# Performance work log

Measured on AMD Instinct MI355X. Metric: run time of the kernel, lower is better.

The kernel has to match this reference:

```python
import jax, jax.numpy as jnp
from jax import lax
import numpy as np

B, S, D = 32, 2048, 512

def setup_inputs() -> dict:
    key = jax.random.key(0)
    ks = jax.random.split(key, 9)
    inv = 1.0 / np.sqrt(D).astype(np.float32)
    return {
        "query": jax.random.normal(ks[0], (B, 1, D), jnp.float32),
        "value": jax.random.normal(ks[1], (B, S, D), jnp.float32),
        "last_alignment_energy": jax.random.uniform(ks[2], (B, S), jnp.float32),
        "conv_w": jax.random.normal(ks[3], (D, 1, 3), jnp.float32) * 0.1,  # Conv1d(1->D,k=3)
        "conv_b": jax.random.normal(ks[4], (D,), jnp.float32) * 0.01,
        "w_q": jax.random.normal(ks[5], (D, D), jnp.float32) * inv,  # applied as x @ w_q
        "w_v": jax.random.normal(ks[6], (D, D), jnp.float32) * inv,
        "bias": jax.random.uniform(ks[7], (D,), jnp.float32, minval=-0.1, maxval=0.1),
        "score_w": jax.random.normal(ks[8], (D,), jnp.float32) * inv,  # score_proj weight (out=1)
        "score_b": jnp.zeros((), jnp.float32),
    }


def reference(query, value, last_alignment_energy, conv_w, conv_b, w_q, w_v, bias, score_w, score_b):
    # location features: Conv1d(1->D, k=3, pad=1) over the previous alignment
    loc = lax.conv_general_dilated(
        last_alignment_energy[:, None, :], conv_w,
        window_strides=(1,), padding=[(1, 1)],
        dimension_numbers=("NCH", "OIH", "NCH"))  # [B, D, S]
    loc = jnp.transpose(loc, (0, 2, 1)) + conv_b  # [B, S, D]

    # additive attention energy: tanh(Wq q + Wv v + loc + b) @ score_w
    hidden = jnp.tanh(query @ w_q + value @ w_v + loc + bias)  # [B, S, D] (query broadcasts over S)
    scores = hidden @ score_w + score_b                          # [B, S]
    align = jax.nn.softmax(scores, axis=-1)                      # [B, S]

    # context = align^T V
    context = jnp.einsum("bs,bsd->bd", align, value)             # [B, D]
    return context, align
```

## Files before the change

### kernel.cpp

```cpp
#include <hip/hip_runtime.h>
#include <hip/hip_bf16.h>

#define B_ 32
#define S_ 2048
#define D_ 512
#define M_ (B_*S_)

typedef __bf16 bf16x8 __attribute__((ext_vector_type(8)));
typedef float  f32x4  __attribute__((ext_vector_type(4)));

__device__ __forceinline__ float tanh_fast(float x){
  float e2 = __expf(2.f * x);
  return 1.f - 2.f * __builtin_amdgcn_rcpf(e2 + 1.f);
}

__global__ void k_prep(const float* __restrict__ wv,
                       unsigned short* __restrict__ wvr,
                       const float* __restrict__ q,
                       const float* __restrict__ wq,
                       const float* __restrict__ bias,
                       float* __restrict__ qp){
  __shared__ float qs[D_];
  __shared__ float red2[2][128];
  int bid = blockIdx.x, t = threadIdx.x;
  if (bid < 128){
    int frag = bid*4 + (t>>6);
    int lane = t & 63;
    int ks = frag >> 5, nt = frag & 31;
    int k0 = ks*32 + (lane>>4)*8;
    int d  = nt*16 + (lane&15);
    bf16x8 v;
    #pragma unroll
    for (int j=0;j<8;++j) v[j] = (__bf16)wv[(k0+j)*D_ + d];
    *reinterpret_cast<uint4*>(wvr + ((size_t)frag*64 + lane)*8) =
        __builtin_bit_cast(uint4, v);
  } else {
    int idx = bid - 128;
    int b = idx >> 2, ch = idx & 3;
    int dl = t & 127, eg = t >> 7;
    int d  = ch*128 + dl;
    for (int e=t; e<D_; e+=256) qs[e] = q[b*D_+e];
    __syncthreads();
    float a = 0.f;
    #pragma unroll 8
    for (int i=0;i<256;++i){
      int e = eg*256 + i;
      a = fmaf(qs[e], wq[(size_t)e*D_+d], a);
    }
    red2[eg][dl] = a;
    __syncthreads();
    if (eg == 0) qp[b*D_+d] = red2[0][dl] + red2[1][dl] + bias[d];
  }
}

__launch_bounds__(256, 2)
__global__ void k_energy(const float* __restrict__ value,
                         const unsigned short* __restrict__ wvr,
                         const float* __restrict__ qp,
                         const float* __restrict__ energy,
                         const float* __restrict__ conv_w,
                         const float* __restrict__ conv_b,
                         const float* __restrict__ score_w,
                         float* __restrict__ sp,
                         float* __restrict__ cpart,
                         float* __restrict__ mArr,
                         float* __restrict__ lArr){
  const int t    = threadIdx.x;
  const int wave = t >> 6;
  const int lane = t & 63;
  const int quad = lane >> 4;
  const int lm   = lane & 15;
  const int row0 = blockIdx.x * 64;
  const int b    = row0 >> 11;
  const int s0   = row0 & (S_-1);

  __shared__ __align__(16) unsigned short As[2][2][4][64][8];

  const int sr  = t >> 2;
  const int so  = t & 3;
  const float* gA = value + (size_t)(row0+sr)*D_ + so*8;
  unsigned short* wA = &As[0][0][sr>>4][so*16 + (sr&15)][0];

  f32x4 acc[4][8];
  #pragma unroll
  for (int mt=0;mt<4;++mt)
    #pragma unroll
    for (int nt=0;nt<8;++nt)
      acc[mt][nt] = (f32x4){0.f,0.f,0.f,0.f};

  const unsigned short* bP = wvr + ((size_t)(wave*8)*64 + lane)*8;

  bf16x8 bcur[8], bnxt[8];
  #pragma unroll
  for (int n=0;n<8;++n)
    bcur[n] = __builtin_bit_cast(bf16x8,
        *reinterpret_cast<const uint4*>(bP + (size_t)n*512));
  {
    f32x4 p0 = *reinterpret_cast<const f32x4*>(gA);
    f32x4 p1 = *reinterpret_cast<const f32x4*>(gA + 4);
    f32x4 p2 = *reinterpret_cast<const f32x4*>(gA + 32);
    f32x4 p3 = *reinterpret_cast<const f32x4*>(gA + 36);
    bf16x8 t0, t1;
    t0[0]=(__bf16)p0[0]; t0[1]=(__bf16)p0[1]; t0[2]=(__bf16)p0[2]; t0[3]=(__bf16)p0[3];
    t0[4]=(__bf16)p1[0]; t0[5]=(__bf16)p1[1]; t0[6]=(__bf16)p1[2]; t0[7]=(__bf16)p1[3];
    t1[0]=(__bf16)p2[0]; t1[1]=(__bf16)p2[1]; t1[2]=(__bf16)p2[2]; t1[3]=(__bf16)p2[3];
    t1[4]=(__bf16)p3[0]; t1[5]=(__bf16)p3[1]; t1[6]=(__bf16)p3[2]; t1[7]=(__bf16)p3[3];
    *reinterpret_cast<uint4*>(wA)        = __builtin_bit_cast(uint4, t0);
    *reinterpret_cast<uint4*>(wA + 2048) = __builtin_bit_cast(uint4, t1);
  }
  __syncthreads();

  for (int p=0; p<8; ++p){
    const int buf = p & 1;
    unsigned short* wAp = wA + (buf^1)*4096;

    f32x4 n0, n1, n2, n3;
    if (p < 7){
      const float* g = gA + (p+1)*64;
      n0 = *reinterpret_cast<const f32x4*>(g);
      n1 = *reinterpret_cast<const f32x4*>(g + 4);
      n2 = *reinterpret_cast<const f32x4*>(g + 32);
      n3 = *reinterpret_cast<const f32x4*>(g + 36);
    }

    #pragma unroll
    for (int n=0;n<8;++n)
      bnxt[n] = __builtin_bit_cast(bf16x8,
          *reinterpret_cast<const uint4*>(bP + (size_t)((2*p+1)*32+n)*512));

    {
      bf16x8 a[4];
      #pragma unroll
      for (int mt=0;mt<4;++mt)
        a[mt] = *reinterpret_cast<const bf16x8*>(&As[buf][0][mt][lane][0]);
      #pragma unroll
      for (int ntl=0;ntl<8;++ntl)
        #pragma unroll
        for (int mt=0;mt<4;++mt)
          acc[mt][ntl] = __builtin_amdgcn_mfma_f32_16x16x32_bf16(a[mt], bcur[ntl], acc[mt][ntl], 0,0,0);
    }

    if (p < 7){
      #pragma unroll
      for (int n=0;n<8;++n)
        bcur[n] = __builtin_bit_cast(bf16x8,
            *reinterpret_cast<const uint4*>(bP + (size_t)((2*p+2)*32+n)*512));
    }

    {
      bf16x8 a[4];
      #pragma unroll
      for (int mt=0;mt<4;++mt)
        a[mt] = *reinterpret_cast<const bf16x8*>(&As[buf][1][mt][lane][0]);
      #pragma unroll
      for (int ntl=0;ntl<8;++ntl)
        #pragma unroll
        for (int mt=0;mt<4;++mt)
          acc[mt][ntl] = __builtin_amdgcn_mfma_f32_16x16x32_bf16(a[mt], bnxt[ntl], acc[mt][ntl], 0,0,0);
    }

    if (p < 7){
      bf16x8 t0, t1;
      t0[0]=(__bf16)n0[0]; t0[1]=(__bf16)n0[1]; t0[2]=(__bf16)n0[2]; t0[3]=(__bf16)n0[3];
      t0[4]=(__bf16)n1[0]; t0[5]=(__bf16)n1[1]; t0[6]=(__bf16)n1[2]; t0[7]=(__bf16)n1[3];
      t1[0]=(__bf16)n2[0]; t1[1]=(__bf16)n2[1]; t1[2]=(__bf16)n2[2]; t1[3]=(__bf16)n2[3];
      t1[4]=(__bf16)n3[0]; t1[5]=(__bf16)n3[1]; t1[6]=(__bf16)n3[2]; t1[7]=(__bf16)n3[3];
      *reinterpret_cast<uint4*>(wAp)        = __builtin_bit_cast(uint4, t0);
      *reinterpret_cast<uint4*>(wAp + 2048) = __builtin_bit_cast(uint4, t1);
    }
    __syncthreads();
  }

  float sw[8], c0[8], c1[8], c2[8], cb[8], qv[8];
  #pragma unroll
  for (int ntl=0; ntl<8; ++ntl){
    int d = wave*128 + ntl*16 + lm;
    sw[ntl] = score_w[d];
    c0[ntl] = conv_w[d*3+0];
    c1[ntl] = conv_w[d*3+1];
    c2[ntl] = conv_w[d*3+2];
    cb[ntl] = conv_b[d];
    qv[ntl] = qp[b*D_+d];
  }
  float* red  = (float*)&As[0][0][0][0][0];
  float* sArr = red + 256;
  float* eArr = red + 320;
  const float* eB = energy + b*S_;
  #pragma unroll
  for (int mt=0; mt<4; ++mt){
    #pragma unroll
    for (int r=0;r<4;++r){
      int sl = mt*16 + quad*4 + r;
      int s  = s0 + sl;
      float em1 = (s > 0)    ? eB[s-1] : 0.f;
      float e0  =              eB[s];
      float ep1 = (s < S_-1) ? eB[s+1] : 0.f;
      float p = 0.f;
      #pragma unroll
      for (int ntl=0; ntl<8; ++ntl){
        float h = acc[mt][ntl][r] + qv[ntl]
                + fmaf(c0[ntl],em1, fmaf(c1[ntl],e0, fmaf(c2[ntl],ep1, cb[ntl])));
        p = fmaf(sw[ntl], tanh_fast(h), p);
      }
      #pragma unroll
      for (int m=1; m<16; m<<=1) p += __shfl_xor(p, m, 64);
      if (lm == 0) red[wave*64 + sl] = p;
    }
  }
  __syncthreads();
  if (t < 64){
    float sv = red[t] + red[64+t] + red[128+t] + red[192+t];
    sp[row0 + t] = sv;
    sArr[t] = sv;
  }
  __syncthreads();

  if (wave == 0){
    float m = sArr[lane];
    #pragma unroll
    for (int mm=1; mm<64; mm<<=1) m = fmaxf(m, __shfl_xor(m, mm, 64));
    float e = __expf(sArr[lane] - m);
    eArr[lane] = e;
    float l = e;
    #pragma unroll
    for (int mm=1; mm<64; mm<<=1) l += __shfl_xor(l, mm, 64);
    if (lane == 0){ mArr[blockIdx.x] = m; lArr[blockIdx.x] = l; }
  }
  __syncthreads();

  float a0 = 0.f, a1 = 0.f;
  const float* vb = value + (size_t)row0*D_;
  #pragma unroll 8
  for (int s2=0; s2<64; ++s2){
    float wgt = eArr[s2];
    a0 = fmaf(wgt, vb[(size_t)s2*D_ + t],       a0);
    a1 = fmaf(wgt, vb[(size_t)s2*D_ + t + 256], a1);
  }
  cpart[(size_t)blockIdx.x*D_ + t]       = a0;
  cpart[(size_t)blockIdx.x*D_ + t + 256] = a1;
}

__global__ void k_final(const float* __restrict__ sp,
                        const float* __restrict__ mArr,
                        const float* __restrict__ lArr,
                        const float* __restrict__ cpart,
                        float* __restrict__ out_align,
                        float* __restrict__ out_ctx){
  int b = blockIdx.x, t = threadIdx.x;
  __shared__ float wArr[32];
  __shared__ float Msh, Lsh;
  if (t < 32){
    float m = mArr[b*32 + t];
    float M = m;
    #pragma unroll
    for (int mm=1; mm<32; mm<<=1) M = fmaxf(M, __shfl_xor(M, mm, 64));
    float w = __expf(m - M);
    float l = lArr[b*32 + t] * w;
    float L = l;
    #pragma unroll
    for (int mm=1; mm<32; mm<<=1) L += __shfl_xor(L, mm, 64);
    wArr[t] = w;
    if (t == 0){ Msh = M; Lsh = L; }
  }
  __syncthreads();
  float M = Msh, invL = 1.f / Lsh;
  #pragma unroll
  for (int i=0;i<8;++i){
    int s = t + i*256;
    out_align[b*S_ + s] = __expf(sp[b*S_ + s] - M) * invL;
  }
  float a0 = 0.f, a1 = 0.f;
  const float* cp = cpart + (size_t)b*32*D_;
  #pragma unroll
  for (int i=0;i<32;++i){
    float w = wArr[i];
    a0 = fmaf(w, cp[(size_t)i*D_ + t],       a0);
    a1 = fmaf(w, cp[(size_t)i*D_ + t + 256], a1);
  }
  out_ctx[b*D_ + t]       = a0 * invL;
  out_ctx[b*D_ + 256 + t] = a1 * invL;
}

extern "C" void kernel_launch(void* const* d_in, const int* in_sizes, int n_in,
                              void* d_out, int out_size, void* d_ws, size_t ws_size,
                              hipStream_t stream){
  const float* query   = (const float*)d_in[0];
  const float* value   = (const float*)d_in[1];
  const float* energy  = (const float*)d_in[2];
  const float* conv_w  = (const float*)d_in[3];
  const float* conv_b  = (const float*)d_in[4];
  const float* w_q     = (const float*)d_in[5];
  const float* w_v     = (const float*)d_in[6];
  const float* bias    = (const float*)d_in[7];
  const float* score_w = (const float*)d_in[8];
  const float* score_b = (const float*)d_in[9];
  (void)score_b;

  char* ws = (char*)d_ws;
  unsigned short* wvr = (unsigned short*)(ws);
  float* qp    = (float*)(ws + (512<<10));
  float* sp    = (float*)(ws + (576<<10));
  float* cpart = (float*)(ws + (832<<10));
  float* mArr  = (float*)(ws + (2880<<10));
  float* lArr  = (float*)(ws + (2884<<10));

  float* out_ctx   = (float*)d_out;
  float* out_align = out_ctx + B_*D_;

  k_prep  <<<dim3(256),   dim3(256), 0, stream>>>(w_v, wvr, query, w_q, bias, qp);
  k_energy<<<dim3(M_/64), dim3(256), 0, stream>>>(value, wvr, qp, energy,
                                                  conv_w, conv_b, score_w,
                                                  sp, cpart, mArr, lArr);
  k_final <<<dim3(B_),    dim3(256), 0, stream>>>(sp, mArr, lArr, cpart,
                                                  out_align, out_ctx);
}
```

Measured before the change: 262.9 us.

## Keep full bf16 value tile in LDS and reuse it for context

```diff
diff --git a/kernel.cpp b/kernel.cpp
--- a/kernel.cpp
+++ b/kernel.cpp
@@ -74,7 +74,10 @@
   const int b    = row0 >> 11;
   const int s0   = row0 & (S_-1);
 
-  __shared__ __align__(16) unsigned short As[2][2][4][64][8];
+  __shared__ __align__(16) unsigned short As[8][2][4][64][8];
+  __shared__ float red[256 + 128];
+  float* sArr = red + 256;
+  float* eArr = red + 320;
 
   const int sr  = t >> 2;
   const int so  = t & 3;
@@ -111,8 +114,7 @@
   __syncthreads();
 
   for (int p=0; p<8; ++p){
-    const int buf = p & 1;
-    unsigned short* wAp = wA + (buf^1)*4096;
+    unsigned short* wAp = wA + (p+1)*4096;
 
     f32x4 n0, n1, n2, n3;
     if (p < 7){
@@ -132,7 +134,7 @@
       bf16x8 a[4];
       #pragma unroll
       for (int mt=0;mt<4;++mt)
-        a[mt] = *reinterpret_cast<const bf16x8*>(&As[buf][0][mt][lane][0]);
+        a[mt] = *reinterpret_cast<const bf16x8*>(&As[p][0][mt][lane][0]);
       #pragma unroll
       for (int ntl=0;ntl<8;++ntl)
         #pragma unroll
@@ -151,7 +153,7 @@
       bf16x8 a[4];
       #pragma unroll
       for (int mt=0;mt<4;++mt)
-        a[mt] = *reinterpret_cast<const bf16x8*>(&As[buf][1][mt][lane][0]);
+        a[mt] = *reinterpret_cast<const bf16x8*>(&As[p][1][mt][lane][0]);
       #pragma unroll
       for (int ntl=0;ntl<8;++ntl)
         #pragma unroll
@@ -182,9 +184,6 @@
     cb[ntl] = conv_b[d];
     qv[ntl] = qp[b*D_+d];
   }
-  float* red  = (float*)&As[0][0][0][0][0];
-  float* sArr = red + 256;
-  float* eArr = red + 320;
   const float* eB = energy + b*S_;
   #pragma unroll
   for (int mt=0; mt<4; ++mt){
@@ -228,16 +227,27 @@
   }
   __syncthreads();
 
-  float a0 = 0.f, a1 = 0.f;
-  const float* vb = value + (size_t)row0*D_;
-  #pragma unroll 8
-  for (int s2=0; s2<64; ++s2){
-    float wgt = eArr[s2];
-    a0 = fmaf(wgt, vb[(size_t)s2*D_ + t],       a0);
-    a1 = fmaf(wgt, vb[(size_t)s2*D_ + t + 256], a1);
-  }
-  cpart[(size_t)blockIdx.x*D_ + t]       = a0;
-  cpart[(size_t)blockIdx.x*D_ + t + 256] = a1;
+  {
+    const int d0 = 2*t;
+    const int pp = d0 >> 6, hh = (d0 >> 5) & 1, oo = (d0 >> 3) & 3, jj = d0 & 7;
+    const unsigned short* vb = &As[pp][hh][0][oo*16][jj];
+    float a0 = 0.f, a1 = 0.f;
+    const int l4 = lane >> 2;
+    for (int i=0; i<16; ++i){
+      int r = (l4 + i) & 15;
+      #pragma unroll
+      for (int mt=0; mt<4; ++mt){
+        float e = eArr[mt*16 + r];
+        unsigned int w = *reinterpret_cast<const unsigned int*>(vb + mt*512 + r*8);
+        float lo = __builtin_bit_cast(float, w << 16);
+        float hi = __builtin_bit_cast(float, w & 0xffff0000u);
+        a0 = fmaf(e, lo, a0);
+        a1 = fmaf(e, hi, a1);
+      }
+    }
+    cpart[(size_t)blockIdx.x*D_ + d0]     = a0;
+    cpart[(size_t)blockIdx.x*D_ + d0 + 1] = a1;
+  }
 }
 
 __global__ void k_final(const float* __restrict__ sp,
```

Measured after the change: 256.2 us. 1.03x faster.
